# Kernel tuning notes

Hardware: AMD Instinct MI355X
Metric: run time of the kernel (lower is better)

The kernel has to match this reference:

```python
import jax, jax.numpy as jnp
import numpy as np
from jax import lax

DIM = 64
DSTATE = 16
EXPAND = 2
DINNER = DIM * EXPAND
DTRANK = (DIM + 15) // 16  # ceil(d_model/16) = 4
B, D, H, W = 1, 24, 24, 24
EPS = 1e-5


def setup_inputs() -> dict:
    key = jax.random.key(0)
    ks = jax.random.split(key, 40)
    def nrm(i, shape, s=0.02):
        return jax.random.normal(ks[i], shape, jnp.float32) * s
    inp = {}
    inp['x'] = jax.random.normal(ks[0], (B, DIM, D, H, W), jnp.float32)
    # three directional view convs + instance-norm affine params
    inp['w1'] = nrm(1, (DIM, DIM, 3, 1, 1)); inp['b1'] = jnp.zeros((DIM,), jnp.float32)
    inp['g1'] = jnp.ones((DIM,), jnp.float32) + nrm(2, (DIM,)); inp['be1'] = nrm(3, (DIM,))
    inp['w2'] = nrm(4, (DIM, DIM, 1, 3, 1)); inp['b2'] = jnp.zeros((DIM,), jnp.float32)
    inp['g2'] = jnp.ones((DIM,), jnp.float32) + nrm(5, (DIM,)); inp['be2'] = nrm(6, (DIM,))
    inp['w3'] = nrm(7, (DIM, DIM, 1, 1, 3)); inp['b3'] = jnp.zeros((DIM,), jnp.float32)
    inp['g3'] = jnp.ones((DIM,), jnp.float32) + nrm(8, (DIM,)); inp['be3'] = nrm(9, (DIM,))
    # MambaUnit layernorm
    inp['ln_w'] = jnp.ones((DIM,), jnp.float32); inp['ln_b'] = jnp.zeros((DIM,), jnp.float32)
    # Mamba params (shared across the three views, as in the source)
    inp['in_proj_w'] = nrm(10, (2 * DINNER, DIM))
    inp['conv_w'] = jnp.ones((DINNER,), jnp.float32) + nrm(11, (DINNER,))  # d_conv=1 depthwise
    inp['conv_b'] = nrm(12, (DINNER,))
    inp['x_proj_w'] = nrm(13, (DTRANK + 2 * DSTATE, DINNER))
    inp['dt_w'] = nrm(14, (DINNER, DTRANK), 0.1)
    inp['dt_b'] = nrm(15, (DINNER,), 0.1)
    inp['A_log'] = jnp.log(jnp.tile(jnp.arange(1, DSTATE + 1, dtype=jnp.float32), (DINNER, 1)))
    inp['D_param'] = jnp.ones((DINNER,), jnp.float32)
    inp['out_proj_w'] = nrm(16, (DIM, DINNER))
    # fusion 1x1x1 conv + instance norm
    inp['wf'] = nrm(17, (DIM, 3 * DIM, 1, 1, 1)); inp['bf'] = jnp.zeros((DIM,), jnp.float32)
    inp['gf'] = jnp.ones((DIM,), jnp.float32) + nrm(18, (DIM,)); inp['bef'] = nrm(19, (DIM,))
    return inp


def silu(x):
    return x * jax.nn.sigmoid(x)


def conv3d(x, w, b, pad):
    out = lax.conv_general_dilated(
        x, w, (1, 1, 1), [(pad[0], pad[0]), (pad[1], pad[1]), (pad[2], pad[2])],
        dimension_numbers=('NCDHW', 'OIDHW', 'NCDHW'))
    return out + b[None, :, None, None, None]


def instance_norm(x, g, b):
    m = x.mean(axis=(2, 3, 4), keepdims=True)
    v = x.var(axis=(2, 3, 4), keepdims=True)  # biased, as in torch InstanceNorm
    return (x - m) / jnp.sqrt(v + EPS) * g[None, :, None, None, None] + b[None, :, None, None, None]


def layer_norm(x, g, b):
    m = x.mean(axis=-1, keepdims=True)
    v = x.var(axis=-1, keepdims=True)
    return (x - m) / jnp.sqrt(v + EPS) * g + b


def mamba(u, in_proj_w, conv_w, conv_b, x_proj_w, dt_w, dt_b, A_log, D_param, out_proj_w):
    # u: (B, L, d_model)
    xz = u @ in_proj_w.T                       # (B, L, 2*DINNER)
    xi, z = jnp.split(xz, 2, axis=-1)
    xi = silu(xi * conv_w + conv_b)            # d_conv=1 depthwise conv == per-channel affine
    xdbl = xi @ x_proj_w.T                     # (B, L, DTRANK + 2*DSTATE)
    dt = xdbl[..., :DTRANK]
    Bm = xdbl[..., DTRANK:DTRANK + DSTATE]
    Cm = xdbl[..., DTRANK + DSTATE:]
    dt = jax.nn.softplus(dt @ dt_w.T + dt_b)   # (B, L, DINNER)
    A = -jnp.exp(A_log)                        # (DINNER, DSTATE)
    dA = jnp.exp(dt[..., None] * A)            # (B, L, DINNER, DSTATE)
    dBx = dt[..., None] * Bm[:, :, None, :] * xi[..., None]
    def comb(c1, c2):
        a1, b1 = c1
        a2, b2 = c2
        return a1 * a2, a2 * b1 + b2
    _, h = lax.associative_scan(comb, (dA, dBx), axis=1)  # h: (B, L, DINNER, DSTATE)
    y = jnp.einsum('blin,bln->bli', h, Cm) + xi * D_param
    y = y * silu(z)
    return y @ out_proj_w.T


def mamba_unit(x5, ln_w, ln_b, mparams):
    Bb, C = x5.shape[:2]
    dims = x5.shape[2:]
    xf = jnp.transpose(x5.reshape(Bb, C, -1), (0, 2, 1))  # (B, L, C)
    xn = layer_norm(xf, ln_w, ln_b)
    y = mamba(xn, *mparams)
    return jnp.transpose(y, (0, 2, 1)).reshape(Bb, C, *dims)


def reference(x, w1, b1, g1, be1, w2, b2, g2, be2, w3, b3, g3, be3, ln_w, ln_b,
              in_proj_w, conv_w, conv_b, x_proj_w, dt_w, dt_b, A_log, D_param, out_proj_w,
              wf, bf, gf, bef):
    mparams = (in_proj_w, conv_w, conv_b, x_proj_w, dt_w, dt_b, A_log, D_param, out_proj_w)
    v1 = jax.nn.relu(instance_norm(conv3d(x, w1, b1, (1, 0, 0)), g1, be1))
    v2 = jax.nn.relu(instance_norm(conv3d(x, w2, b2, (0, 1, 0)), g2, be2))
    v3 = jax.nn.relu(instance_norm(conv3d(x, w3, b3, (0, 0, 1)), g3, be3))
    m1 = mamba_unit(v1, ln_w, ln_b, mparams)
    m2 = mamba_unit(v2, ln_w, ln_b, mparams)
    m3 = mamba_unit(v3, ln_w, ln_b, mparams)
    cat = jnp.concatenate([m1, m2, m3], axis=1)
    out = jax.nn.relu(instance_norm(conv3d(cat, wf, bf, (0, 0, 0)), gf, bef))
    return out
```

## Files before the change

kernel.cpp:

```cpp
#include <hip/hip_runtime.h>

#define LTOT 13824
#define NCH 108
#define CHL 128
#define EPSF 1e-5f

static const size_t OFF_U   = 1024;
static const size_t NU      = (size_t)3*LTOT*64;
static const size_t NXI     = (size_t)3*LTOT*128;
static const size_t NBM     = (size_t)3*LTOT*16;
static const size_t NAG     = (size_t)3*NCH*128*16;
static const size_t OFF_XIT = OFF_U   + NU;
static const size_t OFF_SZT = OFF_XIT + NXI;
static const size_t OFF_DTT = OFF_SZT + NXI;
static const size_t OFF_BMT = OFF_DTT + NXI;
static const size_t OFF_CMT = OFF_BMT + NBM;
static const size_t OFF_W2  = OFF_CMT + NBM;
static const size_t OFF_WT  = OFF_W2 + 24576;
static const size_t OFF_WI  = OFF_WT + 36864;
static const size_t OFF_AGA = OFF_U;
static const size_t OFF_AGB = OFF_U + NAG;
static const size_t OFF_SEED= OFF_U + 2*NAG;
static const size_t OFF_FIN = OFF_DTT;

__device__ __forceinline__ float sigm(float x){ return 1.f/(1.f+__expf(-x)); }
__device__ __forceinline__ float siluf(float x){ return x*sigm(x); }
__device__ __forceinline__ float softplusf(float x){
    return fmaxf(x,0.f) + log1pf(__expf(-fabsf(x)));
}

template<int CTRL>
__device__ __forceinline__ float dpp_add(float x){
    int v = __builtin_amdgcn_update_dpp(0, __float_as_int(x), CTRL, 0xf, 0xf, true);
    return x + __int_as_float(v);
}
__device__ __forceinline__ float sum16(float x){
    x = dpp_add<0xB1>(x);
    x = dpp_add<0x4E>(x);
    x = dpp_add<0x141>(x);
    x = dpp_add<0x140>(x);
    return x;
}

__global__ __launch_bounds__(256) void k_prep(const float* __restrict__ w1,
                      const float* __restrict__ w2, const float* __restrict__ w3,
                      const float* __restrict__ opw, const float* __restrict__ wf,
                      const float* __restrict__ ipw,
                      float* __restrict__ wt, float* __restrict__ w2t,
                      float* __restrict__ wi)
{
    if (blockIdx.x < 144){
        int idx = blockIdx.x*256 + threadIdx.x;
        int r = idx / 12288, rem = idx % 12288;
        int k = rem >> 6, o = rem & 63;
        const float* W = (r==0)?w1:(r==1)?w2:w3;
        wt[idx] = W[o*192 + k];
    } else if (blockIdx.x < 240){
        int idx = (blockIdx.x-144)*256 + threadIdx.x;
        int o = idx & 63, ri = idx >> 6;
        int r = ri >> 7, i = ri & 127;
        float acc = 0.f;
        for (int c2=0;c2<64;c2++)
            acc += opw[c2*128+i] * wf[o*192 + r*64 + c2];
        w2t[idx] = acc;
    } else {
        int idx = (blockIdx.x-240)*256 + threadIdx.x;
        int col = idx & 255, q = idx >> 8;
        wi[q*256 + col] = ipw[col*64 + q];
    }
}

__global__ __launch_bounds__(192) void k_conv(const float* __restrict__ x,
                       const float* __restrict__ wt,
                       const float* __restrict__ b1, const float* __restrict__ b2,
                       const float* __restrict__ b3,
                       float* __restrict__ u, float* __restrict__ ws)
{
    __shared__ __align__(16) float xs[2*1152];
    __shared__ __align__(16) float wl[48*64];
    __shared__ float ssum[64], ssq[64];
    const int r = blockIdx.y;
    const int row0 = blockIdx.x*2;
    const float* Bz = (r==0)?b1:(r==1)?b2:b3;
    const int tid = threadIdx.x;

    if (tid < 64){ ssum[tid]=0.f; ssq[tid]=0.f; }

    const int rw = (tid >= 96) ? 1 : 0, t2 = tid - rw*96;
    const int og = t2 & 15, wg2 = t2 >> 4;
    const int o0 = og*4, w0 = wg2*4;
    float acc[4][4];
    {
        float b0 = Bz[o0], b1v = Bz[o0+1], b2v = Bz[o0+2], b3v = Bz[o0+3];
        #pragma unroll
        for (int wj=0;wj<4;wj++){ acc[0][wj]=b0; acc[1][wj]=b1v; acc[2][wj]=b2v; acc[3][wj]=b3v; }
    }

    const float* wtr = wt + (size_t)r*12288;
    const float* xrow = &xs[rw*1152];
    const int d0 = (row0)/24,   h0 = (row0)%24;
    const int d1 = (row0+1)/24, h1 = (row0+1)%24;

    for (int ph=0; ph<4; ph++){
        __syncthreads();
        for (int s = tid; s < 3072; s += 192)
            wl[s] = wtr[ph*3072 + s];
        for (int rw2=0; rw2<2; rw2++){
            int row = row0 + rw2;
            int d = rw2 ? d1 : d0, h = rw2 ? h1 : h0;
            for (int s = tid; s < 1152; s += 192){
                int w = s % 24; int kt = s / 24; int ic2 = kt/3, t = kt%3;
                int ic = ph*16 + ic2;
                int src = 0; bool valid = true;
                if (r==0){ int dd = d+t-1; valid = (dd>=0 && dd<24); src = (dd*24+h)*24 + w; }
                else if (r==1){ int hh = h+t-1; valid = (hh>=0 && hh<24); src = (d*24+hh)*24 + w; }
                else { int ww = w+t-1; valid = (ww>=0 && ww<24); src = row*24 + ww; }
                xs[rw2*1152 + s] = valid ? x[(size_t)ic*LTOT + src] : 0.f;
            }
        }
        __syncthreads();
        for (int ic2=0; ic2<16; ic2++){
            #pragma unroll
            for (int t=0;t<3;t++){
                float4 wv = *(const float4*)&wl[(ic2*3+t)*64 + o0];
                float4 xv = *(const float4*)&xrow[(ic2*3+t)*24 + w0];
                acc[0][0]=fmaf(wv.x,xv.x,acc[0][0]); acc[0][1]=fmaf(wv.x,xv.y,acc[0][1]);
                acc[0][2]=fmaf(wv.x,xv.z,acc[0][2]); acc[0][3]=fmaf(wv.x,xv.w,acc[0][3]);
                acc[1][0]=fmaf(wv.y,xv.x,acc[1][0]); acc[1][1]=fmaf(wv.y,xv.y,acc[1][1]);
                acc[1][2]=fmaf(wv.y,xv.z,acc[1][2]); acc[1][3]=fmaf(wv.y,xv.w,acc[1][3]);
                acc[2][0]=fmaf(wv.z,xv.x,acc[2][0]); acc[2][1]=fmaf(wv.z,xv.y,acc[2][1]);
                acc[2][2]=fmaf(wv.z,xv.z,acc[2][2]); acc[2][3]=fmaf(wv.z,xv.w,acc[2][3]);
                acc[3][0]=fmaf(wv.w,xv.x,acc[3][0]); acc[3][1]=fmaf(wv.w,xv.y,acc[3][1]);
                acc[3][2]=fmaf(wv.w,xv.z,acc[3][2]); acc[3][3]=fmaf(wv.w,xv.w,acc[3][3]);
            }
        }
    }

    size_t ub = ((size_t)r*LTOT + (size_t)(row0+rw)*24)*64;
    float ps[4]={0,0,0,0}, pq[4]={0,0,0,0};
    #pragma unroll
    for (int wj=0; wj<4; wj++){
        float4 v = make_float4(acc[0][wj],acc[1][wj],acc[2][wj],acc[3][wj]);
        *(float4*)&u[ub + (size_t)(w0+wj)*64 + o0] = v;
        ps[0]+=v.x; pq[0]+=v.x*v.x; ps[1]+=v.y; pq[1]+=v.y*v.y;
        ps[2]+=v.z; pq[2]+=v.z*v.z; ps[3]+=v.w; pq[3]+=v.w*v.w;
    }
    #pragma unroll
    for (int oj=0;oj<4;oj++){
        atomicAdd(&ssum[o0+oj], ps[oj]);
        atomicAdd(&ssq[o0+oj], pq[oj]);
    }
    __syncthreads();
    if (tid < 64){
        atomicAdd(&ws[r*64 + tid], ssum[tid]);
        atomicAdd(&ws[192 + r*64 + tid], ssq[tid]);
    }
}

__global__ __launch_bounds__(192) void k_stats1(float* ws){
    int t = threadIdx.x;
    float s = ws[t], q = ws[192+t];
    float m = s*(1.f/(float)LTOT);
    float v = q*(1.f/(float)LTOT) - m*m;
    ws[512+t] = m; ws[704+t] = rsqrtf(v + EPSF);
}

__global__ __launch_bounds__(256, 4) void k_inproj(const float* __restrict__ u, float* __restrict__ xiT,
                         float* __restrict__ szT, const float* __restrict__ wi,
                         const float* __restrict__ cw, const float* __restrict__ cb,
                         const float* __restrict__ ws,
                         const float* g1,const float* be1,const float* g2,const float* be2,
                         const float* g3,const float* be3,
                         const float* lnw,const float* lnb)
{
    __shared__ float xl[64*65];
    const int tid = threadIdx.x, r = blockIdx.y;
    const int lane = tid & 63;
    const int wv = __builtin_amdgcn_readfirstlane(tid >> 6);
    const int l0 = blockIdx.x*64;
    size_t gbase = (size_t)r*LTOT + l0;

    {
        const float* g  = (r==0)?g1:(r==1)?g2:g3;
        const float* be = (r==0)?be1:(r==1)?be2:be3;
        float m  = ws[512 + r*64 + lane], rs = ws[704 + r*64 + lane];
        float gg = g[lane], bb = be[lane];
        float lw = lnw[lane], lb = lnb[lane];
        for (int j=0;j<16;j++){
            int p = wv*16 + j;
            float vv = u[(gbase+p)*64 + lane];
            vv = fmaxf((vv-m)*rs*gg + bb, 0.f);
            float s1 = sum16(vv), s2 = sum16(vv*vv);
            s1 += __shfl_xor(s1,16); s2 += __shfl_xor(s2,16);
            s1 += __shfl_xor(s1,32); s2 += __shfl_xor(s2,32);
            float mean = s1*(1.f/64.f);
            float var  = s2*(1.f/64.f) - mean*mean;
            xl[lane*65 + p] = (vv-mean)*rsqrtf(var+EPSF)*lw + lb;
        }
    }
    __syncthreads();

    float acc[64];
    #pragma unroll
    for (int j=0;j<64;j++) acc[j] = 0.f;
    const float* wbase = wi + wv*64;
    for (int q=0;q<64;q++){
        float xq = xl[q*65 + lane];
        const float* wq = wbase + q*256;
        #pragma unroll
        for (int j=0;j<64;j++)
            acc[j] = fmaf(wq[j], xq, acc[j]);
    }

    const bool isx = (wv < 2);
    float* dst = isx ? xiT : szT;
    const int c0 = (wv & 1)*64;
    #pragma unroll
    for (int j=0;j<64;j++){
        int c2 = c0 + j;
        float v;
        if (isx) v = siluf(fmaf(acc[j], cw[c2], cb[c2]));
        else     v = siluf(acc[j]);
        dst[((size_t)r*128 + c2)*LTOT + l0 + lane] = v;
    }
}

__global__ __launch_bounds__(256) void k_xproj(const float* __restrict__ xiT, float* __restrict__ dtT,
                        float* __restrict__ BmT, float* __restrict__ CmT,
                        const float* __restrict__ xpw, const float* __restrict__ dtw,
                        const float* __restrict__ dtb)
{
    __shared__ __align__(16) float xt[128*36];
    __shared__ float ww[36*129];
    __shared__ float sd[4*36];
    const int tid = threadIdx.x, r = blockIdx.y;
    const int l0 = blockIdx.x*32;

    for (int s = tid; s < 4096; s += 256){
        int c = s>>5, p = s&31;
        xt[c*36+p] = xiT[((size_t)r*128 + c)*LTOT + l0 + p];
    }
    for (int s = tid; s < 4608; s += 256){
        int k = s>>7, c = s&127;
        ww[k*129+c] = xpw[s];
    }
    __syncthreads();

    const int wv = tid>>6, lane = tid&63;
    float acc[8] = {0,0,0,0,0,0,0,0};
    if (lane < 36){
        const float* wrow = &ww[lane*129];
        for (int c=0;c<128;c++){
            float w = wrow[c];
            float4 a = *(const float4*)&xt[c*36 + wv*8];
            float4 b = *(const float4*)&xt[c*36 + wv*8 + 4];
            acc[0]=fmaf(w,a.x,acc[0]); acc[1]=fmaf(w,a.y,acc[1]);
            acc[2]=fmaf(w,a.z,acc[2]); acc[3]=fmaf(w,a.w,acc[3]);
            acc[4]=fmaf(w,b.x,acc[4]); acc[5]=fmaf(w,b.y,acc[5]);
            acc[6]=fmaf(w,b.z,acc[6]); acc[7]=fmaf(w,b.w,acc[7]);
        }
    }
    if (lane>=4 && lane<36){
        float* dst = (lane<20) ? BmT : CmT;
        int n = (lane<20) ? (lane-4) : (lane-20);
        size_t base = ((size_t)r*16 + n)*LTOT + l0 + wv*8;
        *(float4*)&dst[base]   = make_float4(acc[0],acc[1],acc[2],acc[3]);
        *(float4*)&dst[base+4] = make_float4(acc[4],acc[5],acc[6],acc[7]);
    }
    if (lane < 4){
        #pragma unroll
        for (int p=0;p<8;p++) sd[lane*36 + wv*8 + p] = acc[p];
    }
    __syncthreads();

    const int i = tid>>1, ph = tid&1;
    float4 dw = *(const float4*)&dtw[i*4];
    float db = dtb[i];
    float buf[16];
    #pragma unroll
    for (int t=0;t<16;t++){
        int p = ph*16 + t;
        float v = db + dw.x*sd[0*36+p] + dw.y*sd[1*36+p]
                     + dw.z*sd[2*36+p] + dw.w*sd[3*36+p];
        buf[t] = softplusf(v);
    }
    size_t base = ((size_t)r*128 + i)*LTOT + l0 + ph*16;
    #pragma unroll
    for (int q=0;q<4;q++){
        *(float4*)&dtT[base + 4*q] =
            make_float4(buf[4*q], buf[4*q+1], buf[4*q+2], buf[4*q+3]);
    }
}

__global__ __launch_bounds__(256) void k_scan1(const float* __restrict__ dtT, const float* __restrict__ BmT,
                        const float* __restrict__ xiT, const float* __restrict__ Alog,
                        float* __restrict__ aga, float* __restrict__ agb)
{
    __shared__ __align__(16) float sdt[64*68];
    __shared__ __align__(16) float sxi[64*68];
    __shared__ __align__(16) float sbm[16*68];
    const int tid = threadIdx.x;
    const int ng = tid & 3, il = tid >> 2;
    const int c = blockIdx.x, ib = blockIdx.y, r = blockIdx.z;
    const int i = ib*64 + il;

    float A2[4];
    #pragma unroll
    for (int k=0;k<4;k++) A2[k] = -expf(Alog[i*16 + ng*4 + k]) * 1.44269504f;

    const size_t rowDX = ((size_t)r*128 + ib*64)*LTOT + (size_t)c*CHL;
    const size_t rowB  = ((size_t)r*16)*LTOT + (size_t)c*CHL;

    float b0=0.f,b1=0.f,b2=0.f,b3=0.f, dsum=0.f;

    for (int hh=0; hh<2; hh++){
        __syncthreads();
        const int lb = hh*64;
        for (int f = tid; f < 1024; f += 256){
            int row = f >> 4, t4 = f & 15;
            *(float4*)&sdt[row*68 + t4*4] = *(const float4*)&dtT[rowDX + (size_t)row*LTOT + lb + t4*4];
            *(float4*)&sxi[row*68 + t4*4] = *(const float4*)&xiT[rowDX + (size_t)row*LTOT + lb + t4*4];
        }
        for (int f = tid; f < 256; f += 256){
            int row = f >> 4, t4 = f & 15;
            *(float4*)&sbm[row*68 + t4*4] = *(const float4*)&BmT[rowB + (size_t)row*LTOT + lb + t4*4];
        }
        __syncthreads();

        for (int t4 = 0; t4 < 16; t4++){
            float4 d4 = *(const float4*)&sdt[il*68 + t4*4];
            float4 x4 = *(const float4*)&sxi[il*68 + t4*4];
            float4 B0 = *(const float4*)&sbm[(ng*4+0)*68 + t4*4];
            float4 B1 = *(const float4*)&sbm[(ng*4+1)*68 + t4*4];
            float4 B2 = *(const float4*)&sbm[(ng*4+2)*68 + t4*4];
            float4 B3 = *(const float4*)&sbm[(ng*4+3)*68 + t4*4];
            #define S1Q(dv,xv,c0,c1,c2,c3) { \
                float dx = (dv)*(xv); dsum += (dv); \
                b0 = fmaf(exp2f(A2[0]*(dv)), b0, dx*(c0)); \
                b1 = fmaf(exp2f(A2[1]*(dv)), b1, dx*(c1)); \
                b2 = fmaf(exp2f(A2[2]*(dv)), b2, dx*(c2)); \
                b3 = fmaf(exp2f(A2[3]*(dv)), b3, dx*(c3)); }
            S1Q(d4.x, x4.x, B0.x, B1.x, B2.x, B3.x)
            S1Q(d4.y, x4.y, B0.y, B1.y, B2.y, B3.y)
            S1Q(d4.z, x4.z, B0.z, B1.z, B2.z, B3.z)
            S1Q(d4.w, x4.w, B0.w, B1.w, B2.w, B3.w)
            #undef S1Q
        }
    }

    size_t o = ((size_t)(r*NCH+c)*128 + i)*16 + ng*4;
    *(float4*)&aga[o] = make_float4(exp2f(A2[0]*dsum), exp2f(A2[1]*dsum),
                                    exp2f(A2[2]*dsum), exp2f(A2[3]*dsum));
    *(float4*)&agb[o] = make_float4(b0,b1,b2,b3);
}

__global__ __launch_bounds__(512) void k_scan2(const float* __restrict__ aga, const float* __restrict__ agb,
                        float* __restrict__ seed)
{
    int t = blockIdx.x*512 + threadIdx.x;
    int r = t >> 11, rem = t & 2047;
    float h = 0.f;
    for (int c=0;c<NCH;c++){
        size_t idx = (size_t)(r*NCH+c)*2048 + rem;
        float a = aga[idx], b = agb[idx];
        seed[idx] = h;
        h = fmaf(a, h, b);
    }
}

__global__ __launch_bounds__(256) void k_scan3(const float* __restrict__ dtT, const float* __restrict__ BmT,
                        const float* __restrict__ CmT, const float* __restrict__ xiT,
                        float* __restrict__ szT, const float* __restrict__ Alog,
                        const float* __restrict__ Dp, const float* __restrict__ seed)
{
    __shared__ __align__(16) float sdt[64*68];
    __shared__ __align__(16) float sxi[64*68];
    __shared__ __align__(16) float sbm[16*68];
    __shared__ __align__(16) float scm[16*68];
    const int tid = threadIdx.x;
    const int ng = tid & 3, il = tid >> 2;
    const int c = blockIdx.x, ib = blockIdx.y, r = blockIdx.z;
    const int i = ib*64 + il;

    float A2[4];
    #pragma unroll
    for (int k=0;k<4;k++) A2[k] = -expf(Alog[i*16 + ng*4 + k]) * 1.44269504f;
    const float Dv = Dp[i];

    float4 h4 = *(const float4*)&seed[((size_t)(r*NCH+c)*128 + i)*16 + ng*4];
    float h0=h4.x, h1=h4.y, h2=h4.z, h3=h4.w;

    const size_t rowDX = ((size_t)r*128 + ib*64)*LTOT + (size_t)c*CHL;
    const size_t rowB  = ((size_t)r*16)*LTOT + (size_t)c*CHL;

    for (int hh=0; hh<2; hh++){
        __syncthreads();
        const int lb = hh*64;
        for (int f = tid; f < 1024; f += 256){
            int row = f >> 4, t4 = f & 15;
            *(float4*)&sdt[row*68 + t4*4] = *(const float4*)&dtT[rowDX + (size_t)row*LTOT + lb + t4*4];
            *(float4*)&sxi[row*68 + t4*4] = *(const float4*)&xiT[rowDX + (size_t)row*LTOT + lb + t4*4];
        }
        for (int f = tid; f < 512; f += 256){
            int half = f >> 8, f2 = f & 255;
            int row = f2 >> 4, t4 = f2 & 15;
            if (half == 0)
                *(float4*)&sbm[row*68 + t4*4] = *(const float4*)&BmT[rowB + (size_t)row*LTOT + lb + t4*4];
            else
                *(float4*)&scm[row*68 + t4*4] = *(const float4*)&CmT[rowB + (size_t)row*LTOT + lb + t4*4];
        }
        __syncthreads();

        for (int t4 = 0; t4 < 16; t4++){
            float4 d4 = *(const float4*)&sdt[il*68 + t4*4];
            float4 x4 = *(const float4*)&sxi[il*68 + t4*4];
            float4 B0 = *(const float4*)&sbm[(ng*4+0)*68 + t4*4];
            float4 B1 = *(const float4*)&sbm[(ng*4+1)*68 + t4*4];
            float4 B2 = *(const float4*)&sbm[(ng*4+2)*68 + t4*4];
            float4 B3 = *(const float4*)&sbm[(ng*4+3)*68 + t4*4];
            float4 C0 = *(const float4*)&scm[(ng*4+0)*68 + t4*4];
            float4 C1 = *(const float4*)&scm[(ng*4+1)*68 + t4*4];
            float4 C2 = *(const float4*)&scm[(ng*4+2)*68 + t4*4];
            float4 C3 = *(const float4*)&scm[(ng*4+3)*68 + t4*4];
            float4 y4;
            #define S3Q(dv,xv,b0c,b1c,b2c,b3c,c0c,c1c,c2c,c3c,oy) { \
                float dx = (dv)*(xv); \
                h0 = fmaf(exp2f(A2[0]*(dv)), h0, dx*(b0c)); \
                h1 = fmaf(exp2f(A2[1]*(dv)), h1, dx*(b1c)); \
                h2 = fmaf(exp2f(A2[2]*(dv)), h2, dx*(b2c)); \
                h3 = fmaf(exp2f(A2[3]*(dv)), h3, dx*(b3c)); \
                float p = h0*(c0c); p = fmaf(h1,(c1c),p); \
                p = fmaf(h2,(c2c),p); p = fmaf(h3,(c3c),p); \
                p = dpp_add<0xB1>(p); p = dpp_add<0x4E>(p); \
                oy = fmaf((xv), Dv, p); }
            S3Q(d4.x,x4.x, B0.x,B1.x,B2.x,B3.x, C0.x,C1.x,C2.x,C3.x, y4.x)
            S3Q(d4.y,x4.y, B0.y,B1.y,B2.y,B3.y, C0.y,C1.y,C2.y,C3.y, y4.y)
            S3Q(d4.z,x4.z, B0.z,B1.z,B2.z,B3.z, C0.z,C1.z,C2.z,C3.z, y4.z)
            S3Q(d4.w,x4.w, B0.w,B1.w,B2.w,B3.w, C0.w,C1.w,C2.w,C3.w, y4.w)
            #undef S3Q
            if (ng == 0) *(float4*)&sdt[il*68 + t4*4] = y4;
        }
        __syncthreads();

        for (int f = tid; f < 1024; f += 256){
            int row = f >> 4, t4 = f & 15;
            size_t gidx = rowDX + (size_t)row*LTOT + lb + t4*4;
            float4 yv = *(const float4*)&sdt[row*68 + t4*4];
            float4 s  = *(const float4*)&szT[gidx];
            *(float4*)&szT[gidx] = make_float4(yv.x*s.x, yv.y*s.y, yv.z*s.z, yv.w*s.w);
        }
    }
}

__global__ __launch_bounds__(256, 1) void k_fin(const float* __restrict__ yT, const float* __restrict__ w2t,
                      const float* __restrict__ bfb, float* __restrict__ fin,
                      float* __restrict__ ws)
{
    __shared__ __align__(16) float yl[384*20];
    __shared__ float part[4*16*64];
    __shared__ float ssum[64], ssq[64];
    const int tid = threadIdx.x;
    const int l0 = blockIdx.x*16;
    const int o = tid & 63, sg = tid >> 6;

    for (int f = tid; f < 6144; f += 256){
        int k = f >> 4, p = f & 15;
        yl[k*20 + p] = yT[(size_t)k*LTOT + l0 + p];
    }
    float wreg[96];
    {
        const float* wp = w2t + (size_t)(sg*96)*64 + o;
        #pragma unroll
        for (int j=0;j<96;j++) wreg[j] = wp[(size_t)j*64];
    }
    if (tid < 64){ ssum[tid]=0.f; ssq[tid]=0.f; }
    __syncthreads();

    float acc[16];
    #pragma unroll
    for (int p=0;p<16;p++) acc[p]=0.f;
    const float* ylbase = &yl[sg*96*20];
    #pragma unroll
    for (int j=0;j<96;j++){
        float w = wreg[j];
        const float4* yp4 = (const float4*)&ylbase[j*20];
        float4 a = yp4[0], b = yp4[1], c = yp4[2], d = yp4[3];
        acc[0] =fmaf(w,a.x,acc[0]);  acc[1] =fmaf(w,a.y,acc[1]);
        acc[2] =fmaf(w,a.z,acc[2]);  acc[3] =fmaf(w,a.w,acc[3]);
        acc[4] =fmaf(w,b.x,acc[4]);  acc[5] =fmaf(w,b.y,acc[5]);
        acc[6] =fmaf(w,b.z,acc[6]);  acc[7] =fmaf(w,b.w,acc[7]);
        acc[8] =fmaf(w,c.x,acc[8]);  acc[9] =fmaf(w,c.y,acc[9]);
        acc[10]=fmaf(w,c.z,acc[10]); acc[11]=fmaf(w,c.w,acc[11]);
        acc[12]=fmaf(w,d.x,acc[12]); acc[13]=fmaf(w,d.y,acc[13]);
        acc[14]=fmaf(w,d.z,acc[14]); acc[15]=fmaf(w,d.w,acc[15]);
    }
    #pragma unroll
    for (int p=0;p<16;p++) part[(sg*16+p)*64 + o] = acc[p];
    __syncthreads();

    float bias = bfb[o];
    float ps=0.f, pq=0.f;
    #pragma unroll
    for (int j=0;j<4;j++){
        int p = sg + j*4;
        float s = part[(0*16+p)*64+o] + part[(1*16+p)*64+o]
                + part[(2*16+p)*64+o] + part[(3*16+p)*64+o] + bias;
        fin[(size_t)(l0+p)*64 + o] = s;
        ps += s; pq += s*s;
    }
    atomicAdd(&ssum[o], ps); atomicAdd(&ssq[o], pq);
    __syncthreads();
    if (tid<64){
        atomicAdd(&ws[384+tid], ssum[tid]);
        atomicAdd(&ws[448+tid], ssq[tid]);
    }
}

__global__ __launch_bounds__(64) void k_statsF(float* ws){
    int t = threadIdx.x;
    float s = ws[384+t], q = ws[448+t];
    float m = s*(1.f/(float)LTOT);
    float v = q*(1.f/(float)LTOT) - m*m;
    ws[896+t] = m; ws[960+t] = rsqrtf(v + EPSF);
}

__global__ __launch_bounds__(256) void k_out(const float* __restrict__ fin, const float* __restrict__ ws,
                      const float* __restrict__ gf, const float* __restrict__ bef,
                      float* __restrict__ out)
{
    __shared__ float tl[64*65];
    const int tid = threadIdx.x;
    const int l0 = blockIdx.x*64;
    for (int s=tid; s<4096; s+=256){
        int li = s>>6, o = s&63;
        float v = fin[(size_t)(l0+li)*64 + o];
        v = fmaxf((v - ws[896+o])*ws[960+o]*gf[o] + bef[o], 0.f);
        tl[o*65+li] = v;
    }
    __syncthreads();
    for (int s=tid; s<4096; s+=256){
        int o = s>>6, li = s&63;
        out[(size_t)o*LTOT + l0 + li] = tl[o*65+li];
    }
}

extern "C" void kernel_launch(void* const* d_in, const int* in_sizes, int n_in,
                              void* d_out, int out_size, void* d_ws, size_t ws_size,
                              hipStream_t stream)
{
    const float* X    = (const float*)d_in[0];
    const float* W1   = (const float*)d_in[1];  const float* B1  = (const float*)d_in[2];
    const float* G1   = (const float*)d_in[3];  const float* BE1 = (const float*)d_in[4];
    const float* W2   = (const float*)d_in[5];  const float* B2  = (const float*)d_in[6];
    const float* G2   = (const float*)d_in[7];  const float* BE2 = (const float*)d_in[8];
    const float* W3   = (const float*)d_in[9];  const float* B3  = (const float*)d_in[10];
    const float* G3   = (const float*)d_in[11]; const float* BE3 = (const float*)d_in[12];
    const float* LNW  = (const float*)d_in[13]; const float* LNB = (const float*)d_in[14];
    const float* IPW  = (const float*)d_in[15];
    const float* CW   = (const float*)d_in[16]; const float* CB  = (const float*)d_in[17];
    const float* XPW  = (const float*)d_in[18];
    const float* DTW  = (const float*)d_in[19]; const float* DTB = (const float*)d_in[20];
    const float* ALOG = (const float*)d_in[21]; const float* DP  = (const float*)d_in[22];
    const float* OPW  = (const float*)d_in[23];
    const float* WF   = (const float*)d_in[24]; const float* BF  = (const float*)d_in[25];
    const float* GF   = (const float*)d_in[26]; const float* BEF = (const float*)d_in[27];
    float* ws = (float*)d_ws;

    (void)hipMemsetAsync(d_ws, 0, 2048, stream);

    k_prep  <<<304, 256, 0, stream>>>(W1, W2, W3, OPW, WF, IPW,
                                      ws+OFF_WT, ws+OFF_W2, ws+OFF_WI);
    k_conv  <<<dim3(288,3), 192, 0, stream>>>(X, ws+OFF_WT, B1, B2, B3, ws+OFF_U, ws);
    k_stats1<<<1, 192, 0, stream>>>(ws);
    k_inproj<<<dim3(216,3), 256, 0, stream>>>(ws+OFF_U, ws+OFF_XIT, ws+OFF_SZT,
                                              ws+OFF_WI, CW, CB, ws,
                                              G1,BE1,G2,BE2,G3,BE3, LNW,LNB);
    k_xproj <<<dim3(432,3), 256, 0, stream>>>(ws+OFF_XIT, ws+OFF_DTT, ws+OFF_BMT,
                                              ws+OFF_CMT, XPW, DTW, DTB);
    k_scan1 <<<dim3(NCH,2,3), 256, 0, stream>>>(ws+OFF_DTT, ws+OFF_BMT, ws+OFF_XIT,
                                                ALOG, ws+OFF_AGA, ws+OFF_AGB);
    k_scan2 <<<12, 512, 0, stream>>>(ws+OFF_AGA, ws+OFF_AGB, ws+OFF_SEED);
    k_scan3 <<<dim3(NCH,2,3), 256, 0, stream>>>(ws+OFF_DTT, ws+OFF_BMT, ws+OFF_CMT,
                                                ws+OFF_XIT, ws+OFF_SZT, ALOG, DP,
                                                ws+OFF_SEED);
    k_fin   <<<864, 256, 0, stream>>>(ws+OFF_SZT, ws+OFF_W2, BF, ws+OFF_FIN, ws);
    k_statsF<<<1, 64, 0, stream>>>(ws);
    k_out   <<<216, 256, 0, stream>>>(ws+OFF_FIN, ws, GF, BEF, (float*)d_out);
}
```

Before: 373.8 us.

## Restructure view conv to 64-position tiles with wave-uniform weights and shuffle stats

Rewrites the directional conv kernel so each block handles 64 consecutive positions, with each wave owning 16 output channels and each lane one position. All 64 input channels × 3 taps are staged in shared memory in one pass. Weights are now read directly from global memory at wave-uniform addresses, replacing the shared-memory weight staging. Instance-norm sums are reduced with wave shuffles instead of shared atomics, cutting synchronisation and the per-phase barriers. It relies on a sum16 helper defined elsewhere and uses 48KB of shared memory per block, which may limit occupancy.

```diff
diff --git a/kernel.cpp b/kernel.cpp
--- a/kernel.cpp
+++ b/kernel.cpp
@@ -70,90 +70,68 @@
     }
 }
 
-__global__ __launch_bounds__(192) void k_conv(const float* __restrict__ x,
+__global__ __launch_bounds__(256) void k_conv(const float* __restrict__ x,
                        const float* __restrict__ wt,
                        const float* __restrict__ b1, const float* __restrict__ b2,
                        const float* __restrict__ b3,
                        float* __restrict__ u, float* __restrict__ ws)
 {
-    __shared__ __align__(16) float xs[2*1152];
-    __shared__ __align__(16) float wl[48*64];
-    __shared__ float ssum[64], ssq[64];
+    __shared__ __align__(16) float xs[3*64*64];
+    const int tid = threadIdx.x;
     const int r = blockIdx.y;
-    const int row0 = blockIdx.x*2;
+    const int l0 = blockIdx.x*64;
+    const int lane = tid & 63;
+    const int wv = __builtin_amdgcn_readfirstlane(tid >> 6);
+    const int o0 = wv*16;
+    const int S = (r==0) ? 576 : (r==1) ? 24 : 1;
+
+    for (int f = tid; f < 12288; f += 256){
+        int p = f & 63, ic = (f >> 6) & 63, t = f >> 12;
+        int l = l0 + p;
+        int ax = (r==0) ? (l/576) : (r==1) ? ((l/24)%24) : (l%24);
+        int aa = ax + t - 1;
+        bool valid = (aa >= 0) && (aa < 24);
+        int ls = valid ? (l + (t-1)*S) : l;
+        xs[((t<<6)+ic)*64 + p] = valid ? x[(size_t)ic*LTOT + ls] : 0.f;
+    }
+
     const float* Bz = (r==0)?b1:(r==1)?b2:b3;
-    const int tid = threadIdx.x;
-
-    if (tid < 64){ ssum[tid]=0.f; ssq[tid]=0.f; }
-
-    const int rw = (tid >= 96) ? 1 : 0, t2 = tid - rw*96;
-    const int og = t2 & 15, wg2 = t2 >> 4;
-    const int o0 = og*4, w0 = wg2*4;
-    float acc[4][4];
-    {
-        float b0 = Bz[o0], b1v = Bz[o0+1], b2v = Bz[o0+2], b3v = Bz[o0+3];
+    float acc[16];
+    #pragma unroll
+    for (int j=0;j<16;j++) acc[j] = Bz[o0+j];
+
+    __syncthreads();
+
+    const float* wrow = wt + (size_t)r*12288 + o0;
+    for (int ic=0; ic<64; ic++){
         #pragma unroll
-        for (int wj=0;wj<4;wj++){ acc[0][wj]=b0; acc[1][wj]=b1v; acc[2][wj]=b2v; acc[3][wj]=b3v; }
-    }
-
-    const float* wtr = wt + (size_t)r*12288;
-    const float* xrow = &xs[rw*1152];
-    const int d0 = (row0)/24,   h0 = (row0)%24;
-    const int d1 = (row0+1)/24, h1 = (row0+1)%24;
-
-    for (int ph=0; ph<4; ph++){
-        __syncthreads();
-        for (int s = tid; s < 3072; s += 192)
-            wl[s] = wtr[ph*3072 + s];
-        for (int rw2=0; rw2<2; rw2++){
-            int row = row0 + rw2;
-            int d = rw2 ? d1 : d0, h = rw2 ? h1 : h0;
-            for (int s = tid; s < 1152; s += 192){
-                int w = s % 24; int kt = s / 24; int ic2 = kt/3, t = kt%3;
-                int ic = ph*16 + ic2;
-                int src = 0; bool valid = true;
-                if (r==0){ int dd = d+t-1; valid = (dd>=0 && dd<24); src = (dd*24+h)*24 + w; }
-                else if (r==1){ int hh = h+t-1; valid = (hh>=0 && hh<24); src = (d*24+hh)*24 + w; }
-                else { int ww = w+t-1; valid = (ww>=0 && ww<24); src = row*24 + ww; }
-                xs[rw2*1152 + s] = valid ? x[(size_t)ic*LTOT + src] : 0.f;
-            }
-        }
-        __syncthreads();
-        for (int ic2=0; ic2<16; ic2++){
+        for (int t=0;t<3;t++){
+            float xq = xs[((t<<6)+ic)*64 + lane];
+            const float* wq = wrow + (ic*3+t)*64;
             #pragma unroll
-            for (int t=0;t<3;t++){
-                float4 wv = *(const float4*)&wl[(ic2*3+t)*64 + o0];
-                float4 xv = *(const float4*)&xrow[(ic2*3+t)*24 + w0];
-                acc[0][0]=fmaf(wv.x,xv.x,acc[0][0]); acc[0][1]=fmaf(wv.x,xv.y,acc[0][1]);
-                acc[0][2]=fmaf(wv.x,xv.z,acc[0][2]); acc[0][3]=fmaf(wv.x,xv.w,acc[0][3]);
-                acc[1][0]=fmaf(wv.y,xv.x,acc[1][0]); acc[1][1]=fmaf(wv.y,xv.y,acc[1][1]);
-                acc[1][2]=fmaf(wv.y,xv.z,acc[1][2]); acc[1][3]=fmaf(wv.y,xv.w,acc[1][3]);
-                acc[2][0]=fmaf(wv.z,xv.x,acc[2][0]); acc[2][1]=fmaf(wv.z,xv.y,acc[2][1]);
-                acc[2][2]=fmaf(wv.z,xv.z,acc[2][2]); acc[2][3]=fmaf(wv.z,xv.w,acc[2][3]);
-                acc[3][0]=fmaf(wv.w,xv.x,acc[3][0]); acc[3][1]=fmaf(wv.w,xv.y,acc[3][1]);
-                acc[3][2]=fmaf(wv.w,xv.z,acc[3][2]); acc[3][3]=fmaf(wv.w,xv.w,acc[3][3]);
-            }
-        }
-    }
-
-    size_t ub = ((size_t)r*LTOT + (size_t)(row0+rw)*24)*64;
-    float ps[4]={0,0,0,0}, pq[4]={0,0,0,0};
-    #pragma unroll
-    for (int wj=0; wj<4; wj++){
-        float4 v = make_float4(acc[0][wj],acc[1][wj],acc[2][wj],acc[3][wj]);
-        *(float4*)&u[ub + (size_t)(w0+wj)*64 + o0] = v;
-        ps[0]+=v.x; pq[0]+=v.x*v.x; ps[1]+=v.y; pq[1]+=v.y*v.y;
-        ps[2]+=v.z; pq[2]+=v.z*v.z; ps[3]+=v.w; pq[3]+=v.w*v.w;
-    }
-    #pragma unroll
-    for (int oj=0;oj<4;oj++){
-        atomicAdd(&ssum[o0+oj], ps[oj]);
-        atomicAdd(&ssq[o0+oj], pq[oj]);
-    }
-    __syncthreads();
-    if (tid < 64){
-        atomicAdd(&ws[r*64 + tid], ssum[tid]);
-        atomicAdd(&ws[192 + r*64 + tid], ssq[tid]);
+            for (int j=0;j<16;j++) acc[j] = fmaf(wq[j], xq, acc[j]);
+        }
+    }
+
+    size_t ub = ((size_t)r*LTOT + l0 + lane)*64 + o0;
+    #pragma unroll
+    for (int q=0;q<4;q++)
+        *(float4*)&u[ub + q*4] = make_float4(acc[q*4],acc[q*4+1],acc[q*4+2],acc[q*4+3]);
+
+    float ps[16], pq[16];
+    #pragma unroll
+    for (int j=0;j<16;j++){
+        float a = acc[j];
+        float s = sum16(a);   s += __shfl_xor(s,16);   s += __shfl_xor(s,32);
+        float q2 = sum16(a*a); q2 += __shfl_xor(q2,16); q2 += __shfl_xor(q2,32);
+        ps[j] = s; pq[j] = q2;
+    }
+    if (lane == 0){
+        #pragma unroll
+        for (int j=0;j<16;j++){
+            atomicAdd(&ws[r*64 + o0 + j], ps[j]);
+            atomicAdd(&ws[192 + r*64 + o0 + j], pq[j]);
+        }
     }
 }
 
@@ -570,7 +548,7 @@
 
     k_prep  <<<304, 256, 0, stream>>>(W1, W2, W3, OPW, WF, IPW,
                                       ws+OFF_WT, ws+OFF_W2, ws+OFF_WI);
-    k_conv  <<<dim3(288,3), 192, 0, stream>>>(X, ws+OFF_WT, B1, B2, B3, ws+OFF_U, ws);
+    k_conv  <<<dim3(216,3), 256, 0, stream>>>(X, ws+OFF_WT, B1, B2, B3, ws+OFF_U, ws);
     k_stats1<<<1, 192, 0, stream>>>(ws);
     k_inproj<<<dim3(216,3), 256, 0, stream>>>(ws+OFF_U, ws+OFF_XIT, ws+OFF_SZT,
                                               ws+OFF_WI, CW, CB, ws,
```

Result: slower. 449.6 us (+20.3%).

## Register-tile in_proj GEMM and stream conv weights directly into registers

Applied to the files above, without the earlier changes.

In k_conv, the per-phase shared-memory staging of conv weights is removed. Each thread now loads its 16 float4 weight slices straight from global memory into registers, one sub-block at a time. In k_inproj, the 64-accumulator-per-lane scheme is replaced by an 8-channel x 4-position register tile per thread, processed in two channel halves, with float4 reads from the shared input and float4 global stores. Launch bounds are relaxed to 2 waves per SIMD. The intent is more FMA work per loaded operand and vectorised stores, at the cost of fewer resident waves. The float4 reads at odd row offsets in the 65-stride padded shared array may be misaligned.

```diff
diff --git a/kernel.cpp b/kernel.cpp
--- a/kernel.cpp
+++ b/kernel.cpp
@@ -77,7 +77,6 @@
                        float* __restrict__ u, float* __restrict__ ws)
 {
     __shared__ __align__(16) float xs[2*1152];
-    __shared__ __align__(16) float wl[48*64];
     __shared__ float ssum[64], ssq[64];
     const int r = blockIdx.y;
     const int row0 = blockIdx.x*2;
@@ -96,15 +95,13 @@
         for (int wj=0;wj<4;wj++){ acc[0][wj]=b0; acc[1][wj]=b1v; acc[2][wj]=b2v; acc[3][wj]=b3v; }
     }
 
-    const float* wtr = wt + (size_t)r*12288;
     const float* xrow = &xs[rw*1152];
     const int d0 = (row0)/24,   h0 = (row0)%24;
     const int d1 = (row0+1)/24, h1 = (row0+1)%24;
+    const float* wbase = wt + (size_t)r*12288 + o0;
 
     for (int ph=0; ph<4; ph++){
         __syncthreads();
-        for (int s = tid; s < 3072; s += 192)
-            wl[s] = wtr[ph*3072 + s];
         for (int rw2=0; rw2<2; rw2++){
             int row = row0 + rw2;
             int d = rw2 ? d1 : d0, h = rw2 ? h1 : h0;
@@ -119,11 +116,17 @@
             }
         }
         __syncthreads();
-        for (int ic2=0; ic2<16; ic2++){
+
+        for (int sub=0; sub<3; sub++){
+            const float* wp = wbase + (size_t)(ph*48 + sub*16)*64;
+            float4 wreg[16];
             #pragma unroll
-            for (int t=0;t<3;t++){
-                float4 wv = *(const float4*)&wl[(ic2*3+t)*64 + o0];
-                float4 xv = *(const float4*)&xrow[(ic2*3+t)*24 + w0];
+            for (int kk=0;kk<16;kk++)
+                wreg[kk] = *(const float4*)&wp[(size_t)kk*64];
+            #pragma unroll
+            for (int kk=0;kk<16;kk++){
+                float4 wv = wreg[kk];
+                float4 xv = *(const float4*)&xrow[(sub*16+kk)*24 + w0];
                 acc[0][0]=fmaf(wv.x,xv.x,acc[0][0]); acc[0][1]=fmaf(wv.x,xv.y,acc[0][1]);
                 acc[0][2]=fmaf(wv.x,xv.z,acc[0][2]); acc[0][3]=fmaf(wv.x,xv.w,acc[0][3]);
                 acc[1][0]=fmaf(wv.y,xv.x,acc[1][0]); acc[1][1]=fmaf(wv.y,xv.y,acc[1][1]);
@@ -165,7 +168,7 @@
     ws[512+t] = m; ws[704+t] = rsqrtf(v + EPSF);
 }
 
-__global__ __launch_bounds__(256, 4) void k_inproj(const float* __restrict__ u, float* __restrict__ xiT,
+__global__ __launch_bounds__(256, 2) void k_inproj(const float* __restrict__ u, float* __restrict__ xiT,
                          float* __restrict__ szT, const float* __restrict__ wi,
                          const float* __restrict__ cw, const float* __restrict__ cb,
                          const float* __restrict__ ws,
@@ -200,28 +203,68 @@
     }
     __syncthreads();
 
-    float acc[64];
-    #pragma unroll
-    for (int j=0;j<64;j++) acc[j] = 0.f;
-    const float* wbase = wi + wv*64;
-    for (int q=0;q<64;q++){
-        float xq = xl[q*65 + lane];
-        const float* wq = wbase + q*256;
+    const int pq = tid & 15, oq = tid >> 4;
+    const int p0 = pq*4;
+
+    #pragma unroll 1
+    for (int ch=0; ch<2; ch++){
+        const int c0 = ch*128 + oq*8;
+        float acc[8][4];
         #pragma unroll
-        for (int j=0;j<64;j++)
-            acc[j] = fmaf(wq[j], xq, acc[j]);
-    }
-
-    const bool isx = (wv < 2);
-    float* dst = isx ? xiT : szT;
-    const int c0 = (wv & 1)*64;
-    #pragma unroll
-    for (int j=0;j<64;j++){
-        int c2 = c0 + j;
-        float v;
-        if (isx) v = siluf(fmaf(acc[j], cw[c2], cb[c2]));
-        else     v = siluf(acc[j]);
-        dst[((size_t)r*128 + c2)*LTOT + l0 + lane] = v;
+        for (int oj=0;oj<8;oj++){ acc[oj][0]=0.f; acc[oj][1]=0.f; acc[oj][2]=0.f; acc[oj][3]=0.f; }
+
+        for (int sub=0; sub<8; sub++){
+            float4 wa[8], wb[8];
+            #pragma unroll
+            for (int qq=0;qq<8;qq++){
+                const float* wp = wi + (size_t)(sub*8+qq)*256 + c0;
+                wa[qq] = *(const float4*)wp;
+                wb[qq] = *(const float4*)(wp+4);
+            }
+            #pragma unroll
+            for (int qq=0;qq<8;qq++){
+                float4 x4 = *(const float4*)&xl[(sub*8+qq)*65 + p0];
+                float4 a = wa[qq], b = wb[qq];
+                acc[0][0]=fmaf(a.x,x4.x,acc[0][0]); acc[0][1]=fmaf(a.x,x4.y,acc[0][1]);
+                acc[0][2]=fmaf(a.x,x4.z,acc[0][2]); acc[0][3]=fmaf(a.x,x4.w,acc[0][3]);
+                acc[1][0]=fmaf(a.y,x4.x,acc[1][0]); acc[1][1]=fmaf(a.y,x4.y,acc[1][1]);
+                acc[1][2]=fmaf(a.y,x4.z,acc[1][2]); acc[1][3]=fmaf(a.y,x4.w,acc[1][3]);
+                acc[2][0]=fmaf(a.z,x4.x,acc[2][0]); acc[2][1]=fmaf(a.z,x4.y,acc[2][1]);
+                acc[2][2]=fmaf(a.z,x4.z,acc[2][2]); acc[2][3]=fmaf(a.z,x4.w,acc[2][3]);
+                acc[3][0]=fmaf(a.w,x4.x,acc[3][0]); acc[3][1]=fmaf(a.w,x4.y,acc[3][1]);
+                acc[3][2]=fmaf(a.w,x4.z,acc[3][2]); acc[3][3]=fmaf(a.w,x4.w,acc[3][3]);
+                acc[4][0]=fmaf(b.x,x4.x,acc[4][0]); acc[4][1]=fmaf(b.x,x4.y,acc[4][1]);
+                acc[4][2]=fmaf(b.x,x4.z,acc[4][2]); acc[4][3]=fmaf(b.x,x4.w,acc[4][3]);
+                acc[5][0]=fmaf(b.y,x4.x,acc[5][0]); acc[5][1]=fmaf(b.y,x4.y,acc[5][1]);
+                acc[5][2]=fmaf(b.y,x4.z,acc[5][2]); acc[5][3]=fmaf(b.y,x4.w,acc[5][3]);
+                acc[6][0]=fmaf(b.z,x4.x,acc[6][0]); acc[6][1]=fmaf(b.z,x4.y,acc[6][1]);
+                acc[6][2]=fmaf(b.z,x4.z,acc[6][2]); acc[6][3]=fmaf(b.z,x4.w,acc[6][3]);
+                acc[7][0]=fmaf(b.w,x4.x,acc[7][0]); acc[7][1]=fmaf(b.w,x4.y,acc[7][1]);
+                acc[7][2]=fmaf(b.w,x4.z,acc[7][2]); acc[7][3]=fmaf(b.w,x4.w,acc[7][3]);
+            }
+        }
+
+        if (ch == 0){
+            #pragma unroll
+            for (int oj=0;oj<8;oj++){
+                int c = c0 + oj;
+                float cwv = cw[c], cbv = cb[c];
+                float4 v = make_float4(
+                    siluf(fmaf(acc[oj][0], cwv, cbv)),
+                    siluf(fmaf(acc[oj][1], cwv, cbv)),
+                    siluf(fmaf(acc[oj][2], cwv, cbv)),
+                    siluf(fmaf(acc[oj][3], cwv, cbv)));
+                *(float4*)&xiT[((size_t)r*128 + c)*LTOT + l0 + p0] = v;
+            }
+        } else {
+            #pragma unroll
+            for (int oj=0;oj<8;oj++){
+                int c = c0 - 128 + oj;
+                float4 v = make_float4(siluf(acc[oj][0]), siluf(acc[oj][1]),
+                                       siluf(acc[oj][2]), siluf(acc[oj][3]));
+                *(float4*)&szT[((size_t)r*128 + c)*LTOT + l0 + p0] = v;
+            }
+        }
     }
 }
 
```

Measured after the change: 368.2 us. No clear change (-1.5%).
